# Optimization experiments

Measured on AMD Instinct MI355X. Metric: run time of the kernel, lower is better.

The kernel has to match this reference:

```python
import jax, jax.numpy as jnp
import numpy as np

EPS = 1e-12  # matches torch.nn.functional.normalize default eps


def setup_inputs() -> dict:
    key = jax.random.key(0)
    k1, k2 = jax.random.split(key)
    N = 25
    f = jax.random.normal(k1, (2 ** N,), dtype=jnp.float32)
    P = jax.random.uniform(k2, (N, 2), dtype=jnp.float32)  # learned filter params, torch.rand init
    return {"f": f, "P": P}


def reference(f, P):
    N = P.shape[0]
    # row-wise L2 normalize (torch F.normalize, dim=1)
    norm = jnp.maximum(jnp.linalg.norm(P, axis=1, keepdims=True), EPS)
    Phi = P / norm                                    # [N, 2] scaling filters
    Psi = jnp.stack([Phi[:, 1], -Phi[:, 0]], axis=1)  # [N, 2] wavelet filters

    details = []  # detail coefficients per level, level i has length 2^(N-i-1)
    for i in range(N):
        f2 = f.reshape(-1, 2)          # pairwise view
        details.append(f2 @ Psi[i])    # detail band -> f_hat[2^(N-i-1):2^(N-i)]
        f = f2 @ Phi[i]                # approximation passed to next level

    # f_hat[0] = final approximation; detail of level i occupies [2^(N-i-1), 2^(N-i))
    f_hat = jnp.concatenate([f] + details[::-1])
    return f_hat
```

## Files before the change

kernel.cpp:

```cpp
#include <hip/hip_runtime.h>
#include <hip/hip_bf16.h>


#define CHUNK 16384
#define THREADS 256
#define NBLOCKS ((1 << 25) / CHUNK)

__device__ __forceinline__ void level_params(const float* __restrict__ P, int j,
                                             float& hx, float& hy) {
    float px = P[2 * j], py = P[2 * j + 1];
    float n = fmaxf(sqrtf(px * px + py * py), 1e-12f);
    hx = px / n;
    hy = py / n;
}

__global__ __launch_bounds__(THREADS)
void wave_lvl0_13(const float* __restrict__ f, const float* __restrict__ P,
                  float* __restrict__ out) {
    __shared__ float A[CHUNK / 2];
    __shared__ float B[CHUNK / 4];
    const int tid = threadIdx.x;
    const int blk = blockIdx.x;

    float hx, hy;
    level_params(P, 0, hx, hy);
    const float4* in4 = reinterpret_cast<const float4*>(f) + (size_t)blk * (CHUNK / 4);
    float2* d0out = reinterpret_cast<float2*>(out + (1 << 24) + (size_t)blk * (CHUNK / 2));
    float2* a0lds = reinterpret_cast<float2*>(A);

#pragma unroll
    for (int t = 0; t < CHUNK / 4 / THREADS; ++t) {
        int idx = tid + t * THREADS;
        float4 v = in4[idx];
        float d0 = v.x * hy - v.y * hx;
        float d1 = v.z * hy - v.w * hx;
        float a0 = v.x * hx + v.y * hy;
        float a1 = v.z * hx + v.w * hy;
        d0out[idx] = make_float2(d0, d1);
        a0lds[idx] = make_float2(a0, a1);
    }
    __syncthreads();

    float* cur = A;
    float* nxt = B;
    for (int j = 1; j <= 13; ++j) {
        int p = CHUNK >> (j + 1);
        level_params(P, j, hx, hy);
        float* dout = out + (1 << (24 - j)) + (size_t)blk * p;
        for (int k = tid; k < p; k += THREADS) {
            float x = cur[2 * k], y = cur[2 * k + 1];
            dout[k] = x * hy - y * hx;
            nxt[k]  = x * hx + y * hy;
        }
        __syncthreads();
        float* tmp = cur; cur = nxt; nxt = tmp;
    }

    if (tid == 0) out[blk] = cur[0];
}

__global__ __launch_bounds__(THREADS)
void wave_lvl14_24(const float* __restrict__ P, float* __restrict__ out) {
    __shared__ float A[NBLOCKS];
    __shared__ float B[NBLOCKS / 2];
    const int tid = threadIdx.x;

    for (int k = tid; k < NBLOCKS; k += THREADS) A[k] = out[k];
    __syncthreads();

    float* cur = A;
    float* nxt = B;
    for (int j = 14; j <= 24; ++j) {
        int p = 1 << (24 - j);
        float hx, hy;
        level_params(P, j, hx, hy);
        float* dout = out + p;
        for (int k = tid; k < p; k += THREADS) {
            float x = cur[2 * k], y = cur[2 * k + 1];
            dout[k] = x * hy - y * hx;
            nxt[k]  = x * hx + y * hy;
        }
        __syncthreads();
        float* tmp = cur; cur = nxt; nxt = tmp;
    }
    if (tid == 0) out[0] = cur[0];
}

extern "C" void kernel_launch(void* const* d_in, const int* in_sizes, int n_in,
                              void* d_out, int out_size, void* d_ws, size_t ws_size,
                              hipStream_t stream) {
    const float* f = (const float*)d_in[0];
    const float* P = (const float*)d_in[1];
    float* out = (float*)d_out;

    wave_lvl0_13<<<NBLOCKS, THREADS, 0, stream>>>(f, P, out);
    wave_lvl14_24<<<1, THREADS, 0, stream>>>(P, out);
}
```

Measured before the change: 54.74 us.

## Fuse first three wavelet levels in registers and shrink shared memory

Each thread now loads eight consecutive inputs and computes levels 0, 1 and 2 in registers, writing the detail bands directly to global memory and only the level-2 approximation to shared memory. This removes two rounds of shared-memory round trips and barriers, and cuts LDS use by a factor of four so more blocks can be resident (launch bounds now request 8 waves per EU). The level-1 and level-2 detail stores are narrower (float2 and scalar), and the strided float4 input loads may coalesce less well.

```diff
diff --git a/kernel.cpp b/kernel.cpp
--- a/kernel.cpp
+++ b/kernel.cpp
@@ -14,37 +14,47 @@
     hy = py / n;
 }
 
-__global__ __launch_bounds__(THREADS)
+__global__ __launch_bounds__(THREADS, 8)
 void wave_lvl0_13(const float* __restrict__ f, const float* __restrict__ P,
                   float* __restrict__ out) {
-    __shared__ float A[CHUNK / 2];
-    __shared__ float B[CHUNK / 4];
+    __shared__ float A[CHUNK / 8];
+    __shared__ float B[CHUNK / 16];
     const int tid = threadIdx.x;
     const int blk = blockIdx.x;
 
-    float hx, hy;
-    level_params(P, 0, hx, hy);
+    float hx0, hy0, hx1, hy1, hx2, hy2;
+    level_params(P, 0, hx0, hy0);
+    level_params(P, 1, hx1, hy1);
+    level_params(P, 2, hx2, hy2);
+
     const float4* in4 = reinterpret_cast<const float4*>(f) + (size_t)blk * (CHUNK / 4);
-    float2* d0out = reinterpret_cast<float2*>(out + (1 << 24) + (size_t)blk * (CHUNK / 2));
-    float2* a0lds = reinterpret_cast<float2*>(A);
+    float4* d0out = reinterpret_cast<float4*>(out + (1 << 24) + (size_t)blk * (CHUNK / 2));
+    float2* d1out = reinterpret_cast<float2*>(out + (1 << 23) + (size_t)blk * (CHUNK / 4));
+    float*  d2out = out + (1 << 22) + (size_t)blk * (CHUNK / 8);
 
-#pragma unroll
-    for (int t = 0; t < CHUNK / 4 / THREADS; ++t) {
-        int idx = tid + t * THREADS;
-        float4 v = in4[idx];
-        float d0 = v.x * hy - v.y * hx;
-        float d1 = v.z * hy - v.w * hx;
-        float a0 = v.x * hx + v.y * hy;
-        float a1 = v.z * hx + v.w * hy;
-        d0out[idx] = make_float2(d0, d1);
-        a0lds[idx] = make_float2(a0, a1);
+#pragma unroll 4
+    for (int t = 0; t < CHUNK / 8 / THREADS; ++t) {
+        int g = tid + t * THREADS;
+        float4 u = in4[2 * g];
+        float4 v = in4[2 * g + 1];
+        float d0 = u.x * hy0 - u.y * hx0, a0 = u.x * hx0 + u.y * hy0;
+        float d1 = u.z * hy0 - u.w * hx0, a1 = u.z * hx0 + u.w * hy0;
+        float d2 = v.x * hy0 - v.y * hx0, a2 = v.x * hx0 + v.y * hy0;
+        float d3 = v.z * hy0 - v.w * hx0, a3 = v.z * hx0 + v.w * hy0;
+        d0out[g] = make_float4(d0, d1, d2, d3);
+        float e0 = a0 * hy1 - a1 * hx1, b0 = a0 * hx1 + a1 * hy1;
+        float e1 = a2 * hy1 - a3 * hx1, b1 = a2 * hx1 + a3 * hy1;
+        d1out[g] = make_float2(e0, e1);
+        d2out[g] = b0 * hy2 - b1 * hx2;
+        A[g]     = b0 * hx2 + b1 * hy2;
     }
     __syncthreads();
 
     float* cur = A;
     float* nxt = B;
-    for (int j = 1; j <= 13; ++j) {
+    for (int j = 3; j <= 13; ++j) {
         int p = CHUNK >> (j + 1);
+        float hx, hy;
         level_params(P, j, hx, hy);
         float* dout = out + (1 << (24 - j)) + (size_t)blk * p;
         for (int k = tid; k < p; k += THREADS) {
```

Result: no change. 53.78 us (-1.7%).

## Restructure wavelet as per-wavefront register cascade with shuffles and nontemporal stores

Applied to the files above, without the earlier changes.

The first kernel now gives each 64-lane wavefront 1024 inputs and computes levels 0-9 in registers, using cross-lane shuffles for the later levels instead of LDS buffers and block-wide barriers. The second kernel uses 1024 threads to process the remaining 2^15 approximations in registers, with one barrier and a final single-wavefront shuffle. Detail outputs are written with nontemporal vector stores. This removes LDS traffic and most __syncthreads, and moves more of the level work out of the serial single-block tail kernel. In exchange it adds more partially-active shuffle steps and narrower stores at the small levels.

```diff
diff --git a/kernel.cpp b/kernel.cpp
--- a/kernel.cpp
+++ b/kernel.cpp
@@ -2,9 +2,24 @@
 #include <hip/hip_bf16.h>
 
 
-#define CHUNK 16384
 #define THREADS 256
-#define NBLOCKS ((1 << 25) / CHUNK)
+#define K1_BLOCKS ((1 << 25) / 1024 / 4)
+#define K2THREADS 1024
+
+typedef __attribute__((ext_vector_type(4))) float f4_t;
+typedef __attribute__((ext_vector_type(2))) float f2_t;
+
+__device__ __forceinline__ void nt_store4(float a, float b, float c, float d, float* p) {
+    f4_t t = {a, b, c, d};
+    __builtin_nontemporal_store(t, (f4_t*)p);
+}
+__device__ __forceinline__ void nt_store2(float a, float b, float* p) {
+    f2_t t = {a, b};
+    __builtin_nontemporal_store(t, (f2_t*)p);
+}
+__device__ __forceinline__ void nt_store1(float v, float* p) {
+    __builtin_nontemporal_store(v, p);
+}
 
 __device__ __forceinline__ void level_params(const float* __restrict__ P, int j,
                                              float& hx, float& hy) {
@@ -14,76 +29,132 @@
     hy = py / n;
 }
 
-__global__ __launch_bounds__(THREADS)
-void wave_lvl0_13(const float* __restrict__ f, const float* __restrict__ P,
-                  float* __restrict__ out) {
-    __shared__ float A[CHUNK / 2];
-    __shared__ float B[CHUNK / 4];
-    const int tid = threadIdx.x;
-    const int blk = blockIdx.x;
+__global__ __launch_bounds__(THREADS, 4)
+void wave_k1(const float* __restrict__ f, const float* __restrict__ P,
+             float* __restrict__ out) {
+    const int lane = threadIdx.x & 63;
+    const int wid  = threadIdx.x >> 6;
+    const int wg   = blockIdx.x * 4 + wid;
 
-    float hx, hy;
-    level_params(P, 0, hx, hy);
-    const float4* in4 = reinterpret_cast<const float4*>(f) + (size_t)blk * (CHUNK / 4);
-    float2* d0out = reinterpret_cast<float2*>(out + (1 << 24) + (size_t)blk * (CHUNK / 2));
-    float2* a0lds = reinterpret_cast<float2*>(A);
+    float hx[10], hy[10];
+#pragma unroll
+    for (int j = 0; j < 10; ++j) level_params(P, j, hx[j], hy[j]);
+
+    const float4* in4 = reinterpret_cast<const float4*>(f) + (size_t)wg * 256 + lane * 4;
+    float4 q0 = in4[0], q1 = in4[1], q2 = in4[2], q3 = in4[3];
+
+    float a0 = q0.x*hx[0]+q0.y*hy[0], a1 = q0.z*hx[0]+q0.w*hy[0];
+    float a2 = q1.x*hx[0]+q1.y*hy[0], a3 = q1.z*hx[0]+q1.w*hy[0];
+    float a4 = q2.x*hx[0]+q2.y*hy[0], a5 = q2.z*hx[0]+q2.w*hy[0];
+    float a6 = q3.x*hx[0]+q3.y*hy[0], a7 = q3.z*hx[0]+q3.w*hy[0];
+    {
+        float* b = out + (1 << 24) + wg * 512 + lane * 8;
+        nt_store4(q0.x*hy[0]-q0.y*hx[0], q0.z*hy[0]-q0.w*hx[0],
+                  q1.x*hy[0]-q1.y*hx[0], q1.z*hy[0]-q1.w*hx[0], b);
+        nt_store4(q2.x*hy[0]-q2.y*hx[0], q2.z*hy[0]-q2.w*hx[0],
+                  q3.x*hy[0]-q3.y*hx[0], q3.z*hy[0]-q3.w*hx[0], b + 4);
+    }
+    float b0 = a0*hx[1]+a1*hy[1], b1 = a2*hx[1]+a3*hy[1];
+    float b2 = a4*hx[1]+a5*hy[1], b3 = a6*hx[1]+a7*hy[1];
+    nt_store4(a0*hy[1]-a1*hx[1], a2*hy[1]-a3*hx[1],
+              a4*hy[1]-a5*hx[1], a6*hy[1]-a7*hx[1],
+              out + (1 << 23) + wg * 256 + lane * 4);
+    float c0 = b0*hx[2]+b1*hy[2], c1 = b2*hx[2]+b3*hy[2];
+    nt_store2(b0*hy[2]-b1*hx[2], b2*hy[2]-b3*hx[2],
+              out + (1 << 22) + wg * 128 + lane * 2);
+    nt_store1(c0*hy[3]-c1*hx[3], out + (1 << 21) + wg * 64 + lane);
+    float v = c0*hx[3]+c1*hy[3];
 
 #pragma unroll
-    for (int t = 0; t < CHUNK / 4 / THREADS; ++t) {
-        int idx = tid + t * THREADS;
-        float4 v = in4[idx];
-        float d0 = v.x * hy - v.y * hx;
-        float d1 = v.z * hy - v.w * hx;
-        float a0 = v.x * hx + v.y * hy;
-        float a1 = v.z * hx + v.w * hy;
-        d0out[idx] = make_float2(d0, d1);
-        a0lds[idx] = make_float2(a0, a1);
+    for (int j = 4; j <= 9; ++j) {
+        int p = 1 << (9 - j);
+        float x = __shfl(v, 2 * lane, 64);
+        float y = __shfl(v, 2 * lane + 1, 64);
+        if (lane < p) out[(1 << (24 - j)) + wg * p + lane] = x*hy[j] - y*hx[j];
+        v = x*hx[j] + y*hy[j];
     }
+    if (lane == 0) out[wg] = v;
+}
+
+__global__ __launch_bounds__(K2THREADS)
+void wave_k2(const float* __restrict__ P, float* __restrict__ out) {
+    __shared__ float S[16];
+    const int lane = threadIdx.x & 63;
+    const int w    = threadIdx.x >> 6;
+
+    float hx[15], hy[15];
+#pragma unroll
+    for (int j = 10; j <= 24; ++j) level_params(P, j, hx[j - 10], hy[j - 10]);
+
+    const float4* in4 = reinterpret_cast<const float4*>(out) + w * 512 + lane * 8;
+    float4 q0 = in4[0], q1 = in4[1], q2 = in4[2], q3 = in4[3];
+    float4 q4 = in4[4], q5 = in4[5], q6 = in4[6], q7 = in4[7];
     __syncthreads();
 
-    float* cur = A;
-    float* nxt = B;
-    for (int j = 1; j <= 13; ++j) {
-        int p = CHUNK >> (j + 1);
-        level_params(P, j, hx, hy);
-        float* dout = out + (1 << (24 - j)) + (size_t)blk * p;
-        for (int k = tid; k < p; k += THREADS) {
-            float x = cur[2 * k], y = cur[2 * k + 1];
-            dout[k] = x * hy - y * hx;
-            nxt[k]  = x * hx + y * hy;
-        }
-        __syncthreads();
-        float* tmp = cur; cur = nxt; nxt = tmp;
+    float a0 = q0.x*hx[0]+q0.y*hy[0], a1 = q0.z*hx[0]+q0.w*hy[0];
+    float a2 = q1.x*hx[0]+q1.y*hy[0], a3 = q1.z*hx[0]+q1.w*hy[0];
+    float a4 = q2.x*hx[0]+q2.y*hy[0], a5 = q2.z*hx[0]+q2.w*hy[0];
+    float a6 = q3.x*hx[0]+q3.y*hy[0], a7 = q3.z*hx[0]+q3.w*hy[0];
+    float a8 = q4.x*hx[0]+q4.y*hy[0], a9 = q4.z*hx[0]+q4.w*hy[0];
+    float aA = q5.x*hx[0]+q5.y*hy[0], aB = q5.z*hx[0]+q5.w*hy[0];
+    float aC = q6.x*hx[0]+q6.y*hy[0], aD = q6.z*hx[0]+q6.w*hy[0];
+    float aE = q7.x*hx[0]+q7.y*hy[0], aF = q7.z*hx[0]+q7.w*hy[0];
+    {
+        float* b = out + (1 << 14) + w * 1024 + lane * 16;
+        nt_store4(q0.x*hy[0]-q0.y*hx[0], q0.z*hy[0]-q0.w*hx[0],
+                  q1.x*hy[0]-q1.y*hx[0], q1.z*hy[0]-q1.w*hx[0], b);
+        nt_store4(q2.x*hy[0]-q2.y*hx[0], q2.z*hy[0]-q2.w*hx[0],
+                  q3.x*hy[0]-q3.y*hx[0], q3.z*hy[0]-q3.w*hx[0], b + 4);
+        nt_store4(q4.x*hy[0]-q4.y*hx[0], q4.z*hy[0]-q4.w*hx[0],
+                  q5.x*hy[0]-q5.y*hx[0], q5.z*hy[0]-q5.w*hx[0], b + 8);
+        nt_store4(q6.x*hy[0]-q6.y*hx[0], q6.z*hy[0]-q6.w*hx[0],
+                  q7.x*hy[0]-q7.y*hx[0], q7.z*hy[0]-q7.w*hx[0], b + 12);
     }
+    float b0 = a0*hx[1]+a1*hy[1], b1 = a2*hx[1]+a3*hy[1];
+    float b2 = a4*hx[1]+a5*hy[1], b3 = a6*hx[1]+a7*hy[1];
+    float b4 = a8*hx[1]+a9*hy[1], b5 = aA*hx[1]+aB*hy[1];
+    float b6 = aC*hx[1]+aD*hy[1], b7 = aE*hx[1]+aF*hy[1];
+    {
+        float* b = out + (1 << 13) + w * 512 + lane * 8;
+        nt_store4(a0*hy[1]-a1*hx[1], a2*hy[1]-a3*hx[1],
+                  a4*hy[1]-a5*hx[1], a6*hy[1]-a7*hx[1], b);
+        nt_store4(a8*hy[1]-a9*hx[1], aA*hy[1]-aB*hx[1],
+                  aC*hy[1]-aD*hx[1], aE*hy[1]-aF*hx[1], b + 4);
+    }
+    float c0 = b0*hx[2]+b1*hy[2], c1 = b2*hx[2]+b3*hy[2];
+    float c2 = b4*hx[2]+b5*hy[2], c3 = b6*hx[2]+b7*hy[2];
+    nt_store4(b0*hy[2]-b1*hx[2], b2*hy[2]-b3*hx[2],
+              b4*hy[2]-b5*hx[2], b6*hy[2]-b7*hx[2],
+              out + (1 << 12) + w * 256 + lane * 4);
+    float d0 = c0*hx[3]+c1*hy[3], d1 = c2*hx[3]+c3*hy[3];
+    nt_store2(c0*hy[3]-c1*hx[3], c2*hy[3]-c3*hx[3],
+              out + (1 << 11) + w * 128 + lane * 2);
+    nt_store1(d0*hy[4]-d1*hx[4], out + (1 << 10) + w * 64 + lane);
+    float v = d0*hx[4]+d1*hy[4];
 
-    if (tid == 0) out[blk] = cur[0];
-}
-
-__global__ __launch_bounds__(THREADS)
-void wave_lvl14_24(const float* __restrict__ P, float* __restrict__ out) {
-    __shared__ float A[NBLOCKS];
-    __shared__ float B[NBLOCKS / 2];
-    const int tid = threadIdx.x;
-
-    for (int k = tid; k < NBLOCKS; k += THREADS) A[k] = out[k];
+#pragma unroll
+    for (int j = 15; j <= 20; ++j) {
+        int p = 1 << (20 - j);
+        float x = __shfl(v, 2 * lane, 64);
+        float y = __shfl(v, 2 * lane + 1, 64);
+        if (lane < p) out[(1 << (24 - j)) + w * p + lane] = x*hy[j-10] - y*hx[j-10];
+        v = x*hx[j-10] + y*hy[j-10];
+    }
+    if (lane == 0) S[w] = v;
     __syncthreads();
 
-    float* cur = A;
-    float* nxt = B;
-    for (int j = 14; j <= 24; ++j) {
-        int p = 1 << (24 - j);
-        float hx, hy;
-        level_params(P, j, hx, hy);
-        float* dout = out + p;
-        for (int k = tid; k < p; k += THREADS) {
-            float x = cur[2 * k], y = cur[2 * k + 1];
-            dout[k] = x * hy - y * hx;
-            nxt[k]  = x * hx + y * hy;
+    if (w == 0) {
+        float t = (lane < 16) ? S[lane] : 0.0f;
+#pragma unroll
+        for (int j = 21; j <= 24; ++j) {
+            int p = 1 << (24 - j);
+            float x = __shfl(t, 2 * lane, 64);
+            float y = __shfl(t, 2 * lane + 1, 64);
+            if (lane < p) out[p + lane] = x*hy[j-10] - y*hx[j-10];
+            t = x*hx[j-10] + y*hy[j-10];
         }
-        __syncthreads();
-        float* tmp = cur; cur = nxt; nxt = tmp;
+        if (lane == 0) out[0] = t;
     }
-    if (tid == 0) out[0] = cur[0];
 }
 
 extern "C" void kernel_launch(void* const* d_in, const int* in_sizes, int n_in,
@@ -93,6 +164,6 @@
     const float* P = (const float*)d_in[1];
     float* out = (float*)d_out;
 
-    wave_lvl0_13<<<NBLOCKS, THREADS, 0, stream>>>(f, P, out);
-    wave_lvl14_24<<<1, THREADS, 0, stream>>>(P, out);
+    wave_k1<<<K1_BLOCKS, THREADS, 0, stream>>>(f, P, out);
+    wave_k2<<<1, K2THREADS, 0, stream>>>(P, out);
 }
```

After: 67.73 us. 1.24x slower.
